# Kernel optimization log

Hardware: AMD Instinct MI355X
Metric: run time of the kernel (lower is better)

Reference implementation:

```python
import jax, jax.numpy as jnp
import numpy as np

N_TAPS = 16
BATCH = 64
T = 480000  # 10 s @ 48 kHz, divisible by hop_length=256


def setup_inputs() -> dict:
    key = jax.random.key(0)
    k1, k2 = jax.random.split(key)
    x = jax.random.normal(k1, (BATCH, T), dtype=jnp.float32)
    b = jax.random.normal(k2, (N_TAPS,), dtype=jnp.float32) * 0.1
    return {"x": x, "b": b}


def reference(x, b):
    """Causal FIR filter: y[t] = sum_k b[k] * x[t-k], zero initial state.

    Equivalent to the torch module's per-timestep shift-register loop,
    expressed as one batched 1-D cross-correlation.
    """
    n = b.shape[0]
    # left-pad with n-1 zeros == zero-initialized shift register
    xp = jnp.pad(x, ((0, 0), (n - 1, 0)))[:, None, :]  # [B, 1, T+n-1]
    # lax.conv is cross-correlation; flip taps so w matches y[t]=sum b[k] x[t-k]
    w = b[::-1][None, None, :]  # [out=1, in=1, width=n]
    y = jax.lax.conv_general_dilated(
        xp, w, window_strides=(1,), padding='VALID',
        dimension_numbers=('NCH', 'OIH', 'NCH'))
    return y[:, 0, :]  # [B, T]
```

## Files before the change

kernel.cpp:

```cpp
#include <hip/hip_runtime.h>

#define BATCH 64
#define T 480000
#define T4 (T / 4)
#define NTAPS 16
#define NC (BATCH * T4)

typedef float floatx4 __attribute__((ext_vector_type(4)));

__device__ __forceinline__ void load5(const float* __restrict__ x, int idx,
                                      floatx4 v[5])
{
    const unsigned row  = (unsigned)idx / (unsigned)T4;
    const int      col4 = idx - (int)(row * T4);
    const floatx4* xr   = (const floatx4*)(x + (size_t)row * T);
#pragma unroll
    for (int m = 0; m < 5; ++m) {
        const int c  = col4 - 4 + m;
        const int cc = c < 0 ? 0 : c;
        floatx4 t = xr[cc];
        if (c < 0) t = (floatx4){0.f, 0.f, 0.f, 0.f};
        v[m] = t;
    }
}

__global__ __launch_bounds__(256) void fir_apply_kernel(
    const float* __restrict__ x,
    const float* __restrict__ b,
    float* __restrict__ y)
{
    float tap[NTAPS];
#pragma unroll
    for (int k = 0; k < NTAPS; ++k) tap[k] = b[k];

    const int stride = gridDim.x * blockDim.x;
    int idx = blockIdx.x * blockDim.x + threadIdx.x;
    if (idx >= NC) return;

    floatx4* yv = (floatx4*)y;

    floatx4 v[5];
    load5(x, idx, v);

    for (;;) {
        const int nidx = idx + stride;
        const bool have_next = nidx < NC;

        floatx4 w[5];
        if (have_next) load5(x, nidx, w);

        float s[20];
#pragma unroll
        for (int m = 0; m < 5; ++m) {
            s[4 * m + 0] = v[m].x;
            s[4 * m + 1] = v[m].y;
            s[4 * m + 2] = v[m].z;
            s[4 * m + 3] = v[m].w;
        }

        float acc[4];
#pragma unroll
        for (int j = 0; j < 4; ++j) {
            float a = 0.f;
#pragma unroll
            for (int k = 0; k < NTAPS; ++k) {
                a += tap[k] * s[16 + j - k];
            }
            acc[j] = a;
        }

        floatx4 out = {acc[0], acc[1], acc[2], acc[3]};
        __builtin_nontemporal_store(out, yv + idx);

        if (!have_next) break;
#pragma unroll
        for (int m = 0; m < 5; ++m) v[m] = w[m];
        idx = nidx;
    }
}

extern "C" void kernel_launch(void* const* d_in, const int* in_sizes, int n_in,
                              void* d_out, int out_size, void* d_ws, size_t ws_size,
                              hipStream_t stream)
{
    const float* x = (const float*)d_in[0];
    const float* b = (const float*)d_in[1];
    float* y = (float*)d_out;

    const int block = 256;
    const int grid = 2048;

    fir_apply_kernel<<<grid, block, 0, stream>>>(x, b, y);
}
```

Before: 217.0 us.

## Stage FIR input tiles in LDS via direct global-to-LDS loads

Replaces the grid-stride kernel, where each thread loaded five overlapping float4 vectors from global memory, with a one-tile-per-block design. Each block copies a 512-float4 tile plus a 4-vector halo into shared memory using global_load_lds. Threads then read their overlapping windows from LDS. This cuts the five-fold redundant global and cache traffic for the input. The cost is a much larger grid of short-lived blocks and an extra barrier before compute.

```diff
diff --git a/kernel.cpp b/kernel.cpp
--- a/kernel.cpp
+++ b/kernel.cpp
@@ -4,78 +4,81 @@
 #define T 480000
 #define T4 (T / 4)
 #define NTAPS 16
-#define NC (BATCH * T4)
+#define TILE 512
+#define SEGS 9
+#define LDSC 576
+#define TPR ((T4 + TILE - 1) / TILE)
 
 typedef float floatx4 __attribute__((ext_vector_type(4)));
 
-__device__ __forceinline__ void load5(const float* __restrict__ x, int idx,
-                                      floatx4 v[5])
-{
-    const unsigned row  = (unsigned)idx / (unsigned)T4;
-    const int      col4 = idx - (int)(row * T4);
-    const floatx4* xr   = (const floatx4*)(x + (size_t)row * T);
-#pragma unroll
-    for (int m = 0; m < 5; ++m) {
-        const int c  = col4 - 4 + m;
-        const int cc = c < 0 ? 0 : c;
-        floatx4 t = xr[cc];
-        if (c < 0) t = (floatx4){0.f, 0.f, 0.f, 0.f};
-        v[m] = t;
-    }
-}
-
-__global__ __launch_bounds__(256) void fir_apply_kernel(
+__global__ __launch_bounds__(256) void fir_tile_kernel(
     const float* __restrict__ x,
     const float* __restrict__ b,
     float* __restrict__ y)
 {
+    __shared__ floatx4 lds4[LDSC];
+
+    const int tid  = threadIdx.x;
+    const int lane = tid & 63;
+    const int wave = tid >> 6;
+
+    const int bid = blockIdx.x;
+    const int r   = bid / TPR;
+    const int t   = bid - r * TPR;
+
+    const int    base_c = t * TILE - 4;
+    const float* xrow   = x + (size_t)r * T;
+
+    for (int seg = wave; seg < SEGS; seg += 4) {
+        int c = base_c + seg * 64 + lane;
+        c = c < 0 ? 0 : c;
+        c = c > T4 - 1 ? T4 - 1 : c;
+        const float* gp = xrow + (size_t)c * 4;
+        __builtin_amdgcn_global_load_lds(
+            (const __attribute__((address_space(1))) void*)gp,
+            (__attribute__((address_space(3))) void*)((char*)&lds4[0] + seg * 1024),
+            16, 0, 0);
+    }
+
     float tap[NTAPS];
 #pragma unroll
     for (int k = 0; k < NTAPS; ++k) tap[k] = b[k];
 
-    const int stride = gridDim.x * blockDim.x;
-    int idx = blockIdx.x * blockDim.x + threadIdx.x;
-    if (idx >= NC) return;
+    __syncthreads();
 
-    floatx4* yv = (floatx4*)y;
+    if (t == 0) {
+        if (tid < 4) lds4[tid] = (floatx4){0.f, 0.f, 0.f, 0.f};
+        __syncthreads();
+    }
 
-    floatx4 v[5];
-    load5(x, idx, v);
+    floatx4* yv = (floatx4*)y + (size_t)r * T4;
 
-    for (;;) {
-        const int nidx = idx + stride;
-        const bool have_next = nidx < NC;
-
-        floatx4 w[5];
-        if (have_next) load5(x, nidx, w);
+#pragma unroll
+    for (int p = 0; p < 2; ++p) {
+        const int j  = tid + 256 * p;
+        const int jo = j + 4;
 
         float s[20];
 #pragma unroll
         for (int m = 0; m < 5; ++m) {
-            s[4 * m + 0] = v[m].x;
-            s[4 * m + 1] = v[m].y;
-            s[4 * m + 2] = v[m].z;
-            s[4 * m + 3] = v[m].w;
+            floatx4 v = lds4[jo - 4 + m];
+            s[4 * m + 0] = v.x;
+            s[4 * m + 1] = v.y;
+            s[4 * m + 2] = v.z;
+            s[4 * m + 3] = v.w;
         }
 
-        float acc[4];
+        floatx4 out;
 #pragma unroll
-        for (int j = 0; j < 4; ++j) {
+        for (int q = 0; q < 4; ++q) {
             float a = 0.f;
 #pragma unroll
-            for (int k = 0; k < NTAPS; ++k) {
-                a += tap[k] * s[16 + j - k];
-            }
-            acc[j] = a;
+            for (int k = 0; k < NTAPS; ++k) a += tap[k] * s[16 + q - k];
+            out[q] = a;
         }
 
-        floatx4 out = {acc[0], acc[1], acc[2], acc[3]};
-        __builtin_nontemporal_store(out, yv + idx);
-
-        if (!have_next) break;
-#pragma unroll
-        for (int m = 0; m < 5; ++m) v[m] = w[m];
-        idx = nidx;
+        const int oc = t * TILE + j;
+        if (oc < T4) __builtin_nontemporal_store(out, yv + oc);
     }
 }
 
@@ -87,8 +90,5 @@
     const float* b = (const float*)d_in[1];
     float* y = (float*)d_out;
 
-    const int block = 256;
-    const int grid = 2048;
-
-    fir_apply_kernel<<<grid, block, 0, stream>>>(x, b, y);
+    fir_tile_kernel<<<BATCH * TPR, 256, 0, stream>>>(x, b, y);
 }
```

Result: faster. 212.1 us (-2.3%).
